# Kernel optimization log

Hardware: AMD Instinct MI355X
Metric: run time of the kernel (lower is better)

The kernel has to match this reference:

```python
import jax, jax.numpy as jnp
import numpy as np

N = 10000; IN = 256; HID = 256; Z = 64; NC = 10; E = 320000
GAMMA = -0.5; ZETA = 1.1; TEMP = 0.5  # GlobalArgs.gamma/zeta, AttentionFusion.temperature


def _spmm(row, col, vals, x):
    # sparse [N,N] @ dense [N,D] via gather + segment-sum scatter
    return jax.ops.segment_sum(vals[:, None] * x[col], row, num_segments=N)


def _encode(x, row, col, vals, gcn_W, gcn_b, m1_W, m1_b, m2_W, m2_b, s1_W, s1_b, s2_W, s2_b):
    hidden = jax.nn.relu(_spmm(row, col, vals, x @ gcn_W + gcn_b))  # GCNLayer
    mean = jax.nn.relu(hidden @ m1_W + m1_b) @ m2_W + m2_b
    std = jax.nn.softplus(jax.nn.relu(hidden @ s1_W + s1_b) @ s2_W + s2_b)
    return mean, mean, std  # eval mode: z = x_mean


def _denoise(x, row, col, vals, nb_W, nb_b, sf_W, sf_b, att_W, att_b):
    h1 = jax.nn.relu(x[row] @ nb_W + nb_b)  # nblayers_0 on source feats
    h2 = jax.nn.relu(x[col] @ sf_W + sf_b)  # selflayers_0 on dest feats
    w = jnp.concatenate([h1, h2], axis=1) @ att_W + att_b  # [E,1] log_alpha
    gate = jax.nn.sigmoid(w[:, 0])  # eval-mode hard-concrete
    mask = jnp.clip(gate * (ZETA - GAMMA) + GAMMA, 0.0, 1.0)
    mv = vals * mask
    rowsum = jax.ops.segment_sum(mv, row, num_segments=N) + 1e-10
    d = jnp.clip(rowsum ** -0.5, 0.0, 10.0)
    norm_vals = mv * d[row] * d[col]
    l0 = jnp.mean(jax.nn.sigmoid(w - jnp.log(-GAMMA / ZETA)))
    return norm_vals, l0


def setup_inputs() -> dict:
    key = jax.random.key(0)
    ks = jax.random.split(key, 32)
    w = lambda k, s: jax.random.normal(k, s, jnp.float32) * 0.05
    inp = {}
    inp['x'] = jax.random.normal(ks[0], (N, IN), jnp.float32)
    inp['row'] = jax.random.randint(ks[1], (E,), 0, N)
    inp['col'] = jax.random.randint(ks[2], (E,), 0, N)
    inp['adj_vals'] = jax.random.uniform(ks[3], (E,), jnp.float32)
    inp['gcn_W'] = w(ks[4], (IN, HID)); inp['gcn_b'] = jnp.zeros((HID,), jnp.float32)
    inp['m1_W'] = w(ks[5], (HID, Z)); inp['m1_b'] = jnp.zeros((Z,), jnp.float32)
    inp['m2_W'] = w(ks[6], (Z, Z)); inp['m2_b'] = jnp.zeros((Z,), jnp.float32)
    inp['s1_W'] = w(ks[7], (HID, Z)); inp['s1_b'] = jnp.zeros((Z,), jnp.float32)
    inp['s2_W'] = w(ks[8], (Z, Z)); inp['s2_b'] = jnp.zeros((Z,), jnp.float32)
    inp['nb_W'] = w(ks[9], (IN, HID)); inp['nb_b'] = jnp.zeros((HID,), jnp.float32)
    inp['sf_W'] = w(ks[10], (IN, HID)); inp['sf_b'] = jnp.zeros((HID,), jnp.float32)
    inp['att_W'] = w(ks[11], (2 * HID, 1)); inp['att_b'] = jnp.zeros((1,), jnp.float32)
    inp['f1_W'] = w(ks[12], (Z, 32)); inp['f1_b'] = jnp.zeros((32,), jnp.float32)
    inp['f2_W'] = jnp.zeros((32, 1), jnp.float32)  # att[2].weight.fill_(0.0)
    inp['head_W'] = w(ks[13], (Z, NC)); inp['head_b'] = jnp.zeros((NC,), jnp.float32)
    inp['d1_W'] = w(ks[14], (Z, HID)); inp['d1_b'] = jnp.zeros((HID,), jnp.float32)
    inp['d2_W'] = w(ks[15], (HID, IN)); inp['d2_b'] = jnp.zeros((IN,), jnp.float32)
    return inp


def reference(x, row, col, adj_vals, gcn_W, gcn_b, m1_W, m1_b, m2_W, m2_b, s1_W, s1_b, s2_W, s2_b,
              nb_W, nb_b, sf_W, sf_b, att_W, att_b, f1_W, f1_b, f2_W, head_W, head_b,
              d1_W, d1_b, d2_W, d2_b):
    enc = (gcn_W, gcn_b, m1_W, m1_b, m2_W, m2_b, s1_W, s1_b, s2_W, s2_b)
    # generative view
    z_gen, mu, logstd = _encode(x, row, col, adj_vals, *enc)
    adj_logits = z_gen @ z_gen.T  # vgae_decoder
    # denoised view
    den_vals, l0_loss = _denoise(x, row, col, adj_vals, nb_W, nb_b, sf_W, sf_b, att_W, att_b)
    z_den, _, _ = _encode(x, row, col, den_vals, *enc)
    # attention fusion
    h = jnp.stack([z_gen, z_den], axis=1)  # [N,2,Z]
    score = jnp.tanh(h @ f1_W + f1_b) @ f2_W  # [N,2,1]
    weights = jax.nn.softmax(score / TEMP, axis=1)
    z_fused = jnp.sum(h * weights, axis=1)
    # heads (cluster_proj is identity)
    q_fused = jax.nn.softmax(z_fused @ head_W + head_b, axis=1)
    q_gen = jax.nn.softmax(z_gen @ head_W + head_b, axis=1)
    q_den = jax.nn.softmax(z_den @ head_W + head_b, axis=1)
    recon_den = jax.nn.relu(z_den @ d1_W + d1_b) @ d2_W + d2_b
    return (q_fused, q_gen, q_den, adj_logits, z_fused, mu, logstd, l0_loss, z_den, weights, recon_den)
```

## Files before the change

kernel.cpp:

```cpp
#include <hip/hip_runtime.h>
#include <math.h>

#define NN 10000
#define EE 320000

#define OQF  0LL
#define OQG  100000LL
#define OQD  200000LL
#define OADJ 300000LL
#define OZF  100300000LL
#define OMU  100940000LL
#define OLS  101580000LL
#define OL0  102220000LL
#define OZD  102220001LL
#define OWT  102860001LL
#define OREC 102880001LL

typedef short short8 __attribute__((ext_vector_type(8)));
typedef float f32x4 __attribute__((ext_vector_type(4)));

static __device__ __forceinline__ ushort f2bf(float f) {
  uint u = __float_as_uint(f);
  return (ushort)((u + 0x7fffu + ((u >> 16) & 1u)) >> 16);
}

__global__ __launch_bounds__(256) void k_prep(
    const float* __restrict__ x,
    const float* __restrict__ gcnW, const float* __restrict__ nbW,
    const float* __restrict__ sfW, const float* __restrict__ d2W,
    const float* __restrict__ d1W, const float* __restrict__ m1W,
    const float* __restrict__ s1W, const float* __restrict__ m2W,
    const float* __restrict__ s2W,
    ushort* __restrict__ XB,
    ushort* __restrict__ GWT, ushort* __restrict__ NWT, ushort* __restrict__ SWT,
    ushort* __restrict__ D2T, ushort* __restrict__ D1T, ushort* __restrict__ M1T,
    ushort* __restrict__ S1T, ushort* __restrict__ M2T, ushort* __restrict__ S2T)
{
  const int b = blockIdx.x, tid = threadIdx.x;
  if (b < 2500) {
    const int i = b * 1024 + tid * 4;
    const float4 v = *(const float4*)(x + i);
    ushort4 u;
    u.x = f2bf(v.x); u.y = f2bf(v.y); u.z = f2bf(v.z); u.w = f2bf(v.w);
    *(ushort4*)(XB + i) = u;
    return;
  }
  const int t2 = b - 2500;
  if (t2 < 1024) {
    const int m = t2 >> 8, n = t2 & 255;
    const float* src = (m == 0) ? gcnW : (m == 1) ? nbW : (m == 2) ? sfW : d2W;
    ushort* dst = (m == 0) ? GWT : (m == 1) ? NWT : (m == 2) ? SWT : D2T;
    dst[n * 256 + tid] = f2bf(src[tid * 256 + n]);
  } else if (t2 < 1088) {
    const int local = (t2 - 1024) * 256 + tid;
    const int n = local >> 6, k = local & 63;
    D1T[local] = f2bf(d1W[k * 256 + n]);
  } else if (t2 < 1152) {
    const int n = t2 - 1088;
    M1T[n * 256 + tid] = f2bf(m1W[tid * 64 + n]);
  } else if (t2 < 1216) {
    const int n = t2 - 1152;
    S1T[n * 256 + tid] = f2bf(s1W[tid * 64 + n]);
  } else if (t2 < 1232) {
    const int local = (t2 - 1216) * 256 + tid;
    const int n = local >> 6, k = local & 63;
    M2T[local] = f2bf(m2W[k * 64 + n]);
  } else {
    const int local = (t2 - 1232) * 256 + tid;
    const int n = local >> 6, k = local & 63;
    S2T[local] = f2bf(s2W[k * 64 + n]);
  }
}

__global__ __launch_bounds__(256) void k_gin(
    const ushort* __restrict__ XB,
    const ushort* __restrict__ GWT, const ushort* __restrict__ NWT,
    const ushort* __restrict__ SWT,
    const float* __restrict__ gcnb, const float* __restrict__ nbb,
    const float* __restrict__ sfb, const float* __restrict__ attW,
    ushort* __restrict__ xwb, float* __restrict__ a1, float* __restrict__ a2)
{
  const int sel = blockIdx.y;
  const ushort* WT = (sel == 0) ? GWT : (sel == 1) ? NWT : SWT;
  const float* B = (sel == 0) ? gcnb : (sel == 1) ? nbb : sfb;
  const float* redw = attW + ((sel == 2) ? 256 : 0);
  float* redout = (sel == 1) ? a1 : a2;

  const int tid = threadIdx.x;
  const int wave = tid >> 6, lane = tid & 63;
  const int lr = lane & 15, lk = lane >> 4;
  const int i0 = blockIdx.x * 64;
  const int j0 = wave * 64;

  f32x4 acc[4][4];
#pragma unroll
  for (int ti = 0; ti < 4; ++ti)
#pragma unroll
    for (int tj = 0; tj < 4; ++tj) acc[ti][tj] = (f32x4){0.f, 0.f, 0.f, 0.f};

  const short8 z8 = {0, 0, 0, 0, 0, 0, 0, 0};
  for (int kk = 0; kk < 8; ++kk) {
    short8 a[4], bfr[4];
#pragma unroll
    for (int t = 0; t < 4; ++t) {
      const int ri = i0 + t * 16 + lr;
      a[t] = (ri < NN) ? *(const short8*)(XB + (size_t)ri * 256 + kk * 32 + lk * 8) : z8;
      bfr[t] = *(const short8*)(WT + (size_t)(j0 + t * 16 + lr) * 256 + kk * 32 + lk * 8);
    }
#pragma unroll
    for (int ti = 0; ti < 4; ++ti)
#pragma unroll
      for (int tj = 0; tj < 4; ++tj)
        acc[ti][tj] = __builtin_amdgcn_mfma_f32_16x16x32_bf16(a[ti], bfr[tj], acc[ti][tj], 0, 0, 0);
  }

  if (sel == 0) {
#pragma unroll
    for (int ti = 0; ti < 4; ++ti) {
      const int gi0 = i0 + ti * 16 + lk * 4;
#pragma unroll
      for (int tj = 0; tj < 4; ++tj) {
        const int gj = j0 + tj * 16 + lr;
        const float bv = B[gj];
#pragma unroll
        for (int r = 0; r < 4; ++r) {
          const int gi = gi0 + r;
          if (gi < NN) xwb[(size_t)gi * 256 + gj] = f2bf(acc[ti][tj][r] + bv);
        }
      }
    }
  } else {
    float bw[4], aw[4];
#pragma unroll
    for (int tj = 0; tj < 4; ++tj) {
      const int gj = j0 + tj * 16 + lr;
      bw[tj] = B[gj];
      aw[tj] = redw[gj];
    }
#pragma unroll
    for (int ti = 0; ti < 4; ++ti) {
      const int gi0 = i0 + ti * 16 + lk * 4;
#pragma unroll
      for (int r = 0; r < 4; ++r) {
        float s = 0.f;
#pragma unroll
        for (int tj = 0; tj < 4; ++tj)
          s += fmaxf(acc[ti][tj][r] + bw[tj], 0.f) * aw[tj];
#pragma unroll
        for (int m = 1; m < 16; m <<= 1) s += __shfl_xor(s, m, 64);
        const int gi = gi0 + r;
        if (lr == 0 && gi < NN) atomicAdd(&redout[gi], s);
      }
    }
  }
}

__global__ __launch_bounds__(256) void k_denoise(
    const int* __restrict__ row, const int* __restrict__ col,
    const float* __restrict__ vals, const float* __restrict__ a1,
    const float* __restrict__ a2, const float* __restrict__ attb,
    float4* __restrict__ bk, int* __restrict__ cnt, float* __restrict__ l0acc)
{
  const int e = blockIdx.x * 256 + threadIdx.x;
  const int r = row[e], c = col[e];
  const float w = a1[r] + a2[c] + attb[0];
  const float gate = 1.f / (1.f + expf(-w));
  const float mask = fminf(fmaxf(gate * 1.6f - 0.5f, 0.f), 1.f);
  const float m = vals[e] * mask;
  const int p = atomicAdd(&cnt[r], 1);
  if (p < 64) bk[(size_t)r * 64 + p] = make_float4(__int_as_float(c), vals[e], m, 0.f);
  float part = 1.f / (1.f + expf(-(w + 0.78845736f)));
#pragma unroll
  for (int off = 32; off > 0; off >>= 1) part += __shfl_down(part, off);
  __shared__ float sw[4];
  if ((threadIdx.x & 63) == 0) sw[threadIdx.x >> 6] = part;
  __syncthreads();
  if (threadIdx.x == 0) atomicAdd(l0acc, sw[0] + sw[1] + sw[2] + sw[3]);
}

__global__ __launch_bounds__(256) void k_dinv(
    const float4* __restrict__ bk, const int* __restrict__ cnt,
    float* __restrict__ dinv)
{
  const int tid = threadIdx.x;
  const int r = blockIdx.x * 4 + (tid >> 6);
  const int lane = tid & 63;
  if (r >= NN) return;
  const int m = min(cnt[r], 64);
  float s = (lane < m) ? bk[(size_t)r * 64 + lane].z : 0.f;
#pragma unroll
  for (int off = 32; off > 0; off >>= 1) s += __shfl_xor(s, off, 64);
  if (lane == 0) dinv[r] = fminf(rsqrtf(s + 1e-10f), 10.f);
}

__global__ __launch_bounds__(256) void k_spmm(
    const ushort* __restrict__ xwb, const float4* __restrict__ bk,
    const int* __restrict__ cnt, const float* __restrict__ dinv,
    ushort* __restrict__ h1, ushort* __restrict__ h2)
{
  const int tid = threadIdx.x;
  const int n = blockIdx.x * 2 + (tid >> 7);
  const int c = tid & 127;
  const int m = min(cnt[n], 64);
  const float dr = dinv[n];
  const float4* b = bk + (size_t)n * 64;
  float a10 = 0.f, a11 = 0.f, a20 = 0.f, a21 = 0.f;
  float b10 = 0.f, b11 = 0.f, b20 = 0.f, b21 = 0.f;
  int i = 0;
  for (; i + 2 <= m; i += 2) {
    const float4 e0 = b[i], e1 = b[i + 1];
    const int c0 = __float_as_int(e0.x), c1 = __float_as_int(e1.x);
    const uint u0 = *(const uint*)(xwb + (size_t)c0 * 256 + 2 * c);
    const uint u1 = *(const uint*)(xwb + (size_t)c1 * 256 + 2 * c);
    const float d0 = dr * dinv[c0] * e0.z;
    const float d1 = dr * dinv[c1] * e1.z;
    const float v00 = __uint_as_float(u0 << 16), v01 = __uint_as_float(u0 & 0xffff0000u);
    const float v10 = __uint_as_float(u1 << 16), v11 = __uint_as_float(u1 & 0xffff0000u);
    a10 = fmaf(e0.y, v00, a10); a11 = fmaf(e0.y, v01, a11);
    a20 = fmaf(d0, v00, a20);   a21 = fmaf(d0, v01, a21);
    b10 = fmaf(e1.y, v10, b10); b11 = fmaf(e1.y, v11, b11);
    b20 = fmaf(d1, v10, b20);   b21 = fmaf(d1, v11, b21);
  }
  if (i < m) {
    const float4 e0 = b[i];
    const int c0 = __float_as_int(e0.x);
    const uint u0 = *(const uint*)(xwb + (size_t)c0 * 256 + 2 * c);
    const float d0 = dr * dinv[c0] * e0.z;
    const float v00 = __uint_as_float(u0 << 16), v01 = __uint_as_float(u0 & 0xffff0000u);
    a10 = fmaf(e0.y, v00, a10); a11 = fmaf(e0.y, v01, a11);
    a20 = fmaf(d0, v00, a20);   a21 = fmaf(d0, v01, a21);
  }
  a10 += b10; a11 += b11; a20 += b20; a21 += b21;
  const uint p1 = (uint)f2bf(fmaxf(a10, 0.f)) | ((uint)f2bf(fmaxf(a11, 0.f)) << 16);
  const uint p2 = (uint)f2bf(fmaxf(a20, 0.f)) | ((uint)f2bf(fmaxf(a21, 0.f)) << 16);
  *(uint*)(h1 + (size_t)n * 256 + 2 * c) = p1;
  *(uint*)(h2 + (size_t)n * 256 + 2 * c) = p2;
}

__global__ __launch_bounds__(128) void k_tail(
    const ushort* __restrict__ H1B, const ushort* __restrict__ H2B,
    const ushort* __restrict__ M1T, const ushort* __restrict__ S1T,
    const ushort* __restrict__ M2T, const ushort* __restrict__ S2T,
    const float* __restrict__ m1b, const float* __restrict__ m2b,
    const float* __restrict__ s1b, const float* __restrict__ s2b,
    float* __restrict__ out, float* __restrict__ zden,
    ushort* __restrict__ zbg, ushort* __restrict__ zbd)
{
  const int v = blockIdx.y;
  const ushort* A   = (v == 2) ? H2B : H1B;
  const ushort* W1T = (v == 1) ? S1T : M1T;
  const float*  B1  = (v == 1) ? s1b : m1b;
  const ushort* W2T = (v == 1) ? S2T : M2T;
  const float*  B2  = (v == 1) ? s2b : m2b;

  __shared__ ushort Ts[128][72];
  const int tid = threadIdx.x;
  const int wave = tid >> 6, lane = tid & 63;
  const int lr = lane & 15, lk = lane >> 4;
  const int i0 = blockIdx.x * 128 + wave * 64;
  const short8 z8 = {0, 0, 0, 0, 0, 0, 0, 0};

  f32x4 acc[4][4];
#pragma unroll
  for (int ti = 0; ti < 4; ++ti)
#pragma unroll
    for (int tj = 0; tj < 4; ++tj) acc[ti][tj] = (f32x4){0.f, 0.f, 0.f, 0.f};
  for (int kk = 0; kk < 8; ++kk) {
    short8 a[4], bfr[4];
#pragma unroll
    for (int t = 0; t < 4; ++t) {
      const int ri = i0 + t * 16 + lr;
      a[t] = (ri < NN) ? *(const short8*)(A + (size_t)ri * 256 + kk * 32 + lk * 8) : z8;
      bfr[t] = *(const short8*)(W1T + (size_t)(t * 16 + lr) * 256 + kk * 32 + lk * 8);
    }
#pragma unroll
    for (int ti = 0; ti < 4; ++ti)
#pragma unroll
      for (int tj = 0; tj < 4; ++tj)
        acc[ti][tj] = __builtin_amdgcn_mfma_f32_16x16x32_bf16(a[ti], bfr[tj], acc[ti][tj], 0, 0, 0);
  }
#pragma unroll
  for (int ti = 0; ti < 4; ++ti) {
#pragma unroll
    for (int tj = 0; tj < 4; ++tj) {
      const int cl = tj * 16 + lr;
      const float b1 = B1[cl];
#pragma unroll
      for (int r = 0; r < 4; ++r) {
        const int lrow = wave * 64 + ti * 16 + lk * 4 + r;
        Ts[lrow][cl] = f2bf(fmaxf(acc[ti][tj][r] + b1, 0.f));
      }
    }
  }
  __syncthreads();
  f32x4 acc2[4][4];
#pragma unroll
  for (int ti = 0; ti < 4; ++ti)
#pragma unroll
    for (int tj = 0; tj < 4; ++tj) acc2[ti][tj] = (f32x4){0.f, 0.f, 0.f, 0.f};
  for (int kk = 0; kk < 2; ++kk) {
    short8 a[4], bfr[4];
#pragma unroll
    for (int t = 0; t < 4; ++t) {
      a[t] = *(const short8*)(&Ts[wave * 64 + t * 16 + lr][kk * 32 + lk * 8]);
      bfr[t] = *(const short8*)(W2T + (size_t)(t * 16 + lr) * 64 + kk * 32 + lk * 8);
    }
#pragma unroll
    for (int ti = 0; ti < 4; ++ti)
#pragma unroll
      for (int tj = 0; tj < 4; ++tj)
        acc2[ti][tj] = __builtin_amdgcn_mfma_f32_16x16x32_bf16(a[ti], bfr[tj], acc2[ti][tj], 0, 0, 0);
  }
#pragma unroll
  for (int ti = 0; ti < 4; ++ti) {
    const int gi0 = i0 + ti * 16 + lk * 4;
#pragma unroll
    for (int tj = 0; tj < 4; ++tj) {
      const int gj = tj * 16 + lr;
      const float bv = B2[gj];
#pragma unroll
      for (int r = 0; r < 4; ++r) {
        const int gi = gi0 + r;
        if (gi >= NN) continue;
        float t = acc2[ti][tj][r] + bv;
        if (v == 0) {
          out[OMU + (size_t)gi * 64 + gj] = t;
          zbg[(size_t)gi * 64 + gj] = f2bf(t);
        } else if (v == 1) {
          t = (t > 20.f) ? t : log1pf(expf(t));
          out[OLS + (size_t)gi * 64 + gj] = t;
        } else {
          zden[(size_t)gi * 64 + gj] = t;
          out[OZD + (size_t)gi * 64 + gj] = t;
          zbd[(size_t)gi * 64 + gj] = f2bf(t);
        }
      }
    }
  }
}

__global__ __launch_bounds__(256) void k_post(
    const ushort* __restrict__ ZBG, const ushort* __restrict__ ZBD,
    const float* __restrict__ ZDENW,
    const ushort* __restrict__ D1T, const float* __restrict__ d1b,
    const ushort* __restrict__ D2T, const float* __restrict__ d2b,
    const float* __restrict__ f1W, const float* __restrict__ f1b,
    const float* __restrict__ f2W,
    const float* __restrict__ hW, const float* __restrict__ hb,
    const float* __restrict__ l0acc, float* __restrict__ out)
{
  __shared__ char smraw[64 * 264 * 2];
  const int b = blockIdx.x;
  const int tid = threadIdx.x;
  const short8 z8 = {0, 0, 0, 0, 0, 0, 0, 0};

  if (b < 157) {
    ushort* HS = (ushort*)smraw;
    const int wave = tid >> 6, lane = tid & 63;
    const int lr = lane & 15, lk = lane >> 4;
    const int i0 = b * 64;
    const int j0 = wave * 64;
    f32x4 acc[4][4];
#pragma unroll
    for (int ti = 0; ti < 4; ++ti)
#pragma unroll
      for (int tj = 0; tj < 4; ++tj) acc[ti][tj] = (f32x4){0.f, 0.f, 0.f, 0.f};
    for (int kk = 0; kk < 2; ++kk) {
      short8 a[4], bfr[4];
#pragma unroll
      for (int t = 0; t < 4; ++t) {
        const int ri = i0 + t * 16 + lr;
        a[t] = (ri < NN) ? *(const short8*)(ZBD + (size_t)ri * 64 + kk * 32 + lk * 8) : z8;
        bfr[t] = *(const short8*)(D1T + (size_t)(j0 + t * 16 + lr) * 64 + kk * 32 + lk * 8);
      }
#pragma unroll
      for (int ti = 0; ti < 4; ++ti)
#pragma unroll
        for (int tj = 0; tj < 4; ++tj)
          acc[ti][tj] = __builtin_amdgcn_mfma_f32_16x16x32_bf16(a[ti], bfr[tj], acc[ti][tj], 0, 0, 0);
    }
#pragma unroll
    for (int ti = 0; ti < 4; ++ti) {
      const int rl0 = ti * 16 + lk * 4;
#pragma unroll
      for (int tj = 0; tj < 4; ++tj) {
        const int cl = j0 + tj * 16 + lr;
        const float bv = d1b[cl];
#pragma unroll
        for (int r = 0; r < 4; ++r)
          HS[(rl0 + r) * 264 + cl] = f2bf(fmaxf(acc[ti][tj][r] + bv, 0.f));
      }
    }
    __syncthreads();
#pragma unroll
    for (int ti = 0; ti < 4; ++ti)
#pragma unroll
      for (int tj = 0; tj < 4; ++tj) acc[ti][tj] = (f32x4){0.f, 0.f, 0.f, 0.f};
    for (int kk = 0; kk < 8; ++kk) {
      short8 a[4], bfr[4];
#pragma unroll
      for (int t = 0; t < 4; ++t) {
        a[t] = *(const short8*)(HS + (t * 16 + lr) * 264 + kk * 32 + lk * 8);
        bfr[t] = *(const short8*)(D2T + (size_t)(j0 + t * 16 + lr) * 256 + kk * 32 + lk * 8);
      }
#pragma unroll
      for (int ti = 0; ti < 4; ++ti)
#pragma unroll
        for (int tj = 0; tj < 4; ++tj)
          acc[ti][tj] = __builtin_amdgcn_mfma_f32_16x16x32_bf16(a[ti], bfr[tj], acc[ti][tj], 0, 0, 0);
    }
#pragma unroll
    for (int ti = 0; ti < 4; ++ti) {
      const int gi0 = i0 + ti * 16 + lk * 4;
#pragma unroll
      for (int tj = 0; tj < 4; ++tj) {
        const int gj = j0 + tj * 16 + lr;
        const float bv = d2b[gj];
#pragma unroll
        for (int r = 0; r < 4; ++r) {
          const int gi = gi0 + r;
          if (gi < NN) out[OREC + (size_t)gi * 256 + gj] = acc[ti][tj][r] + bv;
        }
      }
    }
  } else if (b < 197) {
    const int n = (b - 157) * 256 + tid;
    if (n == 0) out[OL0] = l0acc[0] * (1.f / (float)EE);
    if (n >= NN) return;
    const float* zg = out + OMU + (size_t)n * 64;
    const float* zdn = ZDENW + (size_t)n * 64;
    float ag[32], ad[32];
#pragma unroll
    for (int c2 = 0; c2 < 32; ++c2) { const float bb = f1b[c2]; ag[c2] = bb; ad[c2] = bb; }
    for (int l = 0; l < 64; ++l) {
      const float a = zg[l];
      const float d = zdn[l];
#pragma unroll
      for (int c2 = 0; c2 < 32; ++c2) {
        const float w = f1W[l * 32 + c2];
        ag[c2] = fmaf(a, w, ag[c2]);
        ad[c2] = fmaf(d, w, ad[c2]);
      }
    }
    float sg = 0.f, sd = 0.f;
#pragma unroll
    for (int c2 = 0; c2 < 32; ++c2) {
      sg += tanhf(ag[c2]) * f2W[c2];
      sd += tanhf(ad[c2]) * f2W[c2];
    }
    const float e0 = sg * 2.f, e1 = sd * 2.f;
    const float m = fmaxf(e0, e1);
    float w0 = expf(e0 - m), w1 = expf(e1 - m);
    const float inv = 1.f / (w0 + w1);
    w0 *= inv; w1 *= inv;
    float lgf[10], lgg[10], lgd[10];
#pragma unroll
    for (int c = 0; c < 10; ++c) { const float bb = hb[c]; lgf[c] = bb; lgg[c] = bb; lgd[c] = bb; }
    for (int l = 0; l < 64; ++l) {
      const float zgv = zg[l], zdv = zdn[l];
      const float zfv = w0 * zgv + w1 * zdv;
      out[OZF + (size_t)n * 64 + l] = zfv;
#pragma unroll
      for (int c = 0; c < 10; ++c) {
        const float w = hW[l * 10 + c];
        lgf[c] = fmaf(zfv, w, lgf[c]);
        lgg[c] = fmaf(zgv, w, lgg[c]);
        lgd[c] = fmaf(zdv, w, lgd[c]);
      }
    }
#pragma unroll
    for (int h = 0; h < 3; ++h) {
      float* lg = (h == 0) ? lgf : (h == 1) ? lgg : lgd;
      float* q = out + ((h == 0) ? OQF : (h == 1) ? OQG : OQD) + (size_t)n * 10;
      float mm = lg[0];
#pragma unroll
      for (int c = 1; c < 10; ++c) mm = fmaxf(mm, lg[c]);
      float s = 0.f;
#pragma unroll
      for (int c = 0; c < 10; ++c) { lg[c] = expf(lg[c] - mm); s += lg[c]; }
      const float invq = 1.f / s;
#pragma unroll
      for (int c = 0; c < 10; ++c) q[c] = lg[c] * invq;
    }
    out[OWT + (size_t)n * 2 + 0] = w0;
    out[OWT + (size_t)n * 2 + 1] = w1;
  } else {
    const int bb = b - 197;
    const int bi = bb / 79, bj = bb % 79;
    const int wave = tid >> 6, lane = tid & 63;
    const int lr = lane & 15, lk = lane >> 4;
    const int i0 = bi * 128 + (wave >> 1) * 64;
    const int j0 = bj * 128 + (wave & 1) * 64;
    float* zs = (float*)smraw + wave * (16 * 76);
    short8 a[4][2], bfr[4][2];
#pragma unroll
    for (int t = 0; t < 4; ++t) {
      const int ri = i0 + t * 16 + lr;
      const int rj = j0 + t * 16 + lr;
#pragma unroll
      for (int kk = 0; kk < 2; ++kk) {
        a[t][kk] = (ri < NN) ? *(const short8*)(ZBG + (size_t)ri * 64 + kk * 32 + lk * 8) : z8;
        bfr[t][kk] = (rj < NN) ? *(const short8*)(ZBG + (size_t)rj * 64 + kk * 32 + lk * 8) : z8;
      }
    }
    f32x4 acc[4][4];
#pragma unroll
    for (int ti = 0; ti < 4; ++ti)
#pragma unroll
      for (int tj = 0; tj < 4; ++tj) {
        acc[ti][tj] = (f32x4){0.f, 0.f, 0.f, 0.f};
        acc[ti][tj] = __builtin_amdgcn_mfma_f32_16x16x32_bf16(a[ti][0], bfr[tj][0], acc[ti][tj], 0, 0, 0);
        acc[ti][tj] = __builtin_amdgcn_mfma_f32_16x16x32_bf16(a[ti][1], bfr[tj][1], acc[ti][tj], 0, 0, 0);
      }
#pragma unroll
    for (int ti = 0; ti < 4; ++ti) {
#pragma unroll
      for (int tj = 0; tj < 4; ++tj)
#pragma unroll
        for (int r = 0; r < 4; ++r)
          zs[(lk * 4 + r) * 76 + tj * 16 + lr] = acc[ti][tj][r];
#pragma unroll
      for (int s = 0; s < 4; ++s) {
        const int rrow = (s & 1) * 8 + (lane >> 3);
        const int ccol = (s >> 1) * 32 + (lane & 7) * 4;
        const int gi = i0 + ti * 16 + rrow;
        const int gj = j0 + ccol;
        if (gi < NN && gj < NN) {
          float4 v;
          v.x = zs[rrow * 76 + ccol + 0];
          v.y = zs[rrow * 76 + ccol + 1];
          v.z = zs[rrow * 76 + ccol + 2];
          v.w = zs[rrow * 76 + ccol + 3];
          *(float4*)(out + OADJ + (size_t)gi * NN + gj) = v;
        }
      }
    }
  }
}

extern "C" void kernel_launch(void* const* d_in, const int* in_sizes, int n_in,
                              void* d_out, int out_size, void* d_ws, size_t ws_size,
                              hipStream_t stream)
{
  const float* x     = (const float*)d_in[0];
  const int*   row   = (const int*)d_in[1];
  const int*   col   = (const int*)d_in[2];
  const float* avals = (const float*)d_in[3];
  const float* gcnW  = (const float*)d_in[4];
  const float* gcnb  = (const float*)d_in[5];
  const float* m1W   = (const float*)d_in[6];
  const float* m1b   = (const float*)d_in[7];
  const float* m2W   = (const float*)d_in[8];
  const float* m2b   = (const float*)d_in[9];
  const float* s1W   = (const float*)d_in[10];
  const float* s1b   = (const float*)d_in[11];
  const float* s2W   = (const float*)d_in[12];
  const float* s2b   = (const float*)d_in[13];
  const float* nbW   = (const float*)d_in[14];
  const float* nbb   = (const float*)d_in[15];
  const float* sfW   = (const float*)d_in[16];
  const float* sfb   = (const float*)d_in[17];
  const float* attW  = (const float*)d_in[18];
  const float* attb  = (const float*)d_in[19];
  const float* f1W   = (const float*)d_in[20];
  const float* f1b   = (const float*)d_in[21];
  const float* f2W   = (const float*)d_in[22];
  const float* headW = (const float*)d_in[23];
  const float* headb = (const float*)d_in[24];
  const float* d1W   = (const float*)d_in[25];
  const float* d1b   = (const float*)d_in[26];
  const float* d2W   = (const float*)d_in[27];
  const float* d2b   = (const float*)d_in[28];
  float* out = (float*)d_out;

  float* ws = (float*)d_ws;
  size_t o = 0;
  float4* BK   = (float4*)(ws + o); o += (size_t)NN * 64 * 4;
  ushort* XB   = (ushort*)(ws + o); o += (size_t)NN * 128;
  ushort* XWB  = (ushort*)(ws + o); o += (size_t)NN * 128;
  ushort* GWT  = (ushort*)(ws + o); o += 32768;
  ushort* NWT  = (ushort*)(ws + o); o += 32768;
  ushort* SWT  = (ushort*)(ws + o); o += 32768;
  ushort* D2T  = (ushort*)(ws + o); o += 32768;
  ushort* D1T  = (ushort*)(ws + o); o += 8192;
  ushort* M1T  = (ushort*)(ws + o); o += 8192;
  ushort* S1T  = (ushort*)(ws + o); o += 8192;
  ushort* M2T  = (ushort*)(ws + o); o += 2048;
  ushort* S2T  = (ushort*)(ws + o); o += 2048;
  ushort* H1B  = (ushort*)(ws + o); o += (size_t)NN * 128;
  ushort* H2B  = (ushort*)(ws + o); o += (size_t)NN * 128;
  float* ZDENW = ws + o; o += (size_t)NN * 64;
  ushort* ZBG  = (ushort*)(ws + o); o += (size_t)NN * 32;
  ushort* ZBD  = (ushort*)(ws + o); o += (size_t)NN * 32;
  float* DINV  = ws + o; o += NN;
  const size_t zoff = o;
  float* A1    = ws + o; o += NN;
  float* A2    = ws + o; o += NN;
  int*   CNT   = (int*)(ws + o); o += NN;
  float* L0A   = ws + o; o += 1;

  hipMemsetAsync((void*)(ws + zoff), 0, (o - zoff) * sizeof(float), stream);

  k_prep<<<3748, 256, 0, stream>>>(x, gcnW, nbW, sfW, d2W, d1W, m1W, s1W, m2W, s2W,
                                   XB, GWT, NWT, SWT, D2T, D1T, M1T, S1T, M2T, S2T);
  k_gin<<<dim3(157, 3), 256, 0, stream>>>(XB, GWT, NWT, SWT, gcnb, nbb, sfb, attW, XWB, A1, A2);
  k_denoise<<<EE / 256, 256, 0, stream>>>(row, col, avals, A1, A2, attb, BK, CNT, L0A);
  k_dinv<<<2500, 256, 0, stream>>>(BK, CNT, DINV);
  k_spmm<<<NN / 2, 256, 0, stream>>>(XWB, BK, CNT, DINV, H1B, H2B);
  k_tail<<<dim3(79, 3), 128, 0, stream>>>(H1B, H2B, M1T, S1T, M2T, S2T,
                                          m1b, m2b, s1b, s2b, out, ZDENW, ZBG, ZBD);
  k_post<<<6438, 256, 0, stream>>>(ZBG, ZBD, ZDENW, D1T, d1b, D2T, d2b,
                                   f1W, f1b, f2W, headW, headb, L0A, out);
}
```

Before: 283.0 us.

## Stream adj_logits by row strips with direct MFMA stores; fold memset into prep

The z·zᵀ decoder tile path is rewritten. Each block now owns a 16-row strip and its four waves sweep across all column tiles, writing MFMA accumulators straight to global memory instead of staging them through shared memory for float4 stores. The block count for that path drops from about 6241 to 625. The separate hipMemsetAsync of the accumulator region is replaced by extra zeroing blocks in k_prep, which saves one launch. The direct stores are scalar and strided per lane, which may hurt write coalescing on the 400MB output, and zero-padding checks were removed since 10000 divides by 16.

Result: slower. 308.9 us (+9.2%).

```diff
diff --git a/kernel.cpp b/kernel.cpp
--- a/kernel.cpp
+++ b/kernel.cpp
@@ -34,7 +34,8 @@
     ushort* __restrict__ XB,
     ushort* __restrict__ GWT, ushort* __restrict__ NWT, ushort* __restrict__ SWT,
     ushort* __restrict__ D2T, ushort* __restrict__ D1T, ushort* __restrict__ M1T,
-    ushort* __restrict__ S1T, ushort* __restrict__ M2T, ushort* __restrict__ S2T)
+    ushort* __restrict__ S1T, ushort* __restrict__ M2T, ushort* __restrict__ S2T,
+    float* __restrict__ ZRG)
 {
   const int b = blockIdx.x, tid = threadIdx.x;
   if (b < 2500) {
@@ -65,10 +66,13 @@
     const int local = (t2 - 1216) * 256 + tid;
     const int n = local >> 6, k = local & 63;
     M2T[local] = f2bf(m2W[k * 64 + n]);
-  } else {
+  } else if (t2 < 1248) {
     const int local = (t2 - 1232) * 256 + tid;
     const int n = local >> 6, k = local & 63;
     S2T[local] = f2bf(s2W[k * 64 + n]);
+  } else {
+    const int i = (t2 - 1248) * 1024 + tid * 4;
+    *(float4*)(ZRG + i) = make_float4(0.f, 0.f, 0.f, 0.f);
   }
 }
 
@@ -349,13 +353,12 @@
     const float* __restrict__ hW, const float* __restrict__ hb,
     const float* __restrict__ l0acc, float* __restrict__ out)
 {
-  __shared__ char smraw[64 * 264 * 2];
+  __shared__ ushort HS[64 * 264];
   const int b = blockIdx.x;
   const int tid = threadIdx.x;
   const short8 z8 = {0, 0, 0, 0, 0, 0, 0, 0};
 
   if (b < 157) {
-    ushort* HS = (ushort*)smraw;
     const int wave = tid >> 6, lane = tid & 63;
     const int lr = lane & 15, lk = lane >> 4;
     const int i0 = b * 64;
@@ -485,55 +488,25 @@
     out[OWT + (size_t)n * 2 + 0] = w0;
     out[OWT + (size_t)n * 2 + 1] = w1;
   } else {
-    const int bb = b - 197;
-    const int bi = bb / 79, bj = bb % 79;
+    const int bi = b - 197;
     const int wave = tid >> 6, lane = tid & 63;
     const int lr = lane & 15, lk = lane >> 4;
-    const int i0 = bi * 128 + (wave >> 1) * 64;
-    const int j0 = bj * 128 + (wave & 1) * 64;
-    float* zs = (float*)smraw + wave * (16 * 76);
-    short8 a[4][2], bfr[4][2];
-#pragma unroll
-    for (int t = 0; t < 4; ++t) {
-      const int ri = i0 + t * 16 + lr;
-      const int rj = j0 + t * 16 + lr;
-#pragma unroll
-      for (int kk = 0; kk < 2; ++kk) {
-        a[t][kk] = (ri < NN) ? *(const short8*)(ZBG + (size_t)ri * 64 + kk * 32 + lk * 8) : z8;
-        bfr[t][kk] = (rj < NN) ? *(const short8*)(ZBG + (size_t)rj * 64 + kk * 32 + lk * 8) : z8;
-      }
-    }
-    f32x4 acc[4][4];
-#pragma unroll
-    for (int ti = 0; ti < 4; ++ti)
-#pragma unroll
-      for (int tj = 0; tj < 4; ++tj) {
-        acc[ti][tj] = (f32x4){0.f, 0.f, 0.f, 0.f};
-        acc[ti][tj] = __builtin_amdgcn_mfma_f32_16x16x32_bf16(a[ti][0], bfr[tj][0], acc[ti][tj], 0, 0, 0);
-        acc[ti][tj] = __builtin_amdgcn_mfma_f32_16x16x32_bf16(a[ti][1], bfr[tj][1], acc[ti][tj], 0, 0, 0);
-      }
-#pragma unroll
-    for (int ti = 0; ti < 4; ++ti) {
-#pragma unroll
-      for (int tj = 0; tj < 4; ++tj)
-#pragma unroll
-        for (int r = 0; r < 4; ++r)
-          zs[(lk * 4 + r) * 76 + tj * 16 + lr] = acc[ti][tj][r];
-#pragma unroll
-      for (int s = 0; s < 4; ++s) {
-        const int rrow = (s & 1) * 8 + (lane >> 3);
-        const int ccol = (s >> 1) * 32 + (lane & 7) * 4;
-        const int gi = i0 + ti * 16 + rrow;
-        const int gj = j0 + ccol;
-        if (gi < NN && gj < NN) {
-          float4 v;
-          v.x = zs[rrow * 76 + ccol + 0];
-          v.y = zs[rrow * 76 + ccol + 1];
-          v.z = zs[rrow * 76 + ccol + 2];
-          v.w = zs[rrow * 76 + ccol + 3];
-          *(float4*)(out + OADJ + (size_t)gi * NN + gj) = v;
-        }
-      }
+    const int i0 = bi * 16;
+    const short8 a0 = *(const short8*)(ZBG + (size_t)(i0 + lr) * 64 + lk * 8);
+    const short8 a1 = *(const short8*)(ZBG + (size_t)(i0 + lr) * 64 + 32 + lk * 8);
+    float* crow = out + OADJ + (size_t)(i0 + lk * 4) * NN + lr;
+#pragma unroll 2
+    for (int jt = wave; jt < 625; jt += 4) {
+      const int j0 = jt * 16;
+      const short8 b0 = *(const short8*)(ZBG + (size_t)(j0 + lr) * 64 + lk * 8);
+      const short8 b1 = *(const short8*)(ZBG + (size_t)(j0 + lr) * 64 + 32 + lk * 8);
+      f32x4 acc = (f32x4){0.f, 0.f, 0.f, 0.f};
+      acc = __builtin_amdgcn_mfma_f32_16x16x32_bf16(a0, b0, acc, 0, 0, 0);
+      acc = __builtin_amdgcn_mfma_f32_16x16x32_bf16(a1, b1, acc, 0, 0, 0);
+      crow[(size_t)0 * NN + j0] = acc[0];
+      crow[(size_t)1 * NN + j0] = acc[1];
+      crow[(size_t)2 * NN + j0] = acc[2];
+      crow[(size_t)3 * NN + j0] = acc[3];
     }
   }
 }
@@ -593,22 +566,21 @@
   ushort* ZBG  = (ushort*)(ws + o); o += (size_t)NN * 32;
   ushort* ZBD  = (ushort*)(ws + o); o += (size_t)NN * 32;
   float* DINV  = ws + o; o += NN;
-  const size_t zoff = o;
+  float* ZRG   = ws + o;
   float* A1    = ws + o; o += NN;
   float* A2    = ws + o; o += NN;
   int*   CNT   = (int*)(ws + o); o += NN;
   float* L0A   = ws + o; o += 1;
-
-  hipMemsetAsync((void*)(ws + zoff), 0, (o - zoff) * sizeof(float), stream);
-
-  k_prep<<<3748, 256, 0, stream>>>(x, gcnW, nbW, sfW, d2W, d1W, m1W, s1W, m2W, s2W,
-                                   XB, GWT, NWT, SWT, D2T, D1T, M1T, S1T, M2T, S2T);
+  o += 719;
+
+  k_prep<<<3778, 256, 0, stream>>>(x, gcnW, nbW, sfW, d2W, d1W, m1W, s1W, m2W, s2W,
+                                   XB, GWT, NWT, SWT, D2T, D1T, M1T, S1T, M2T, S2T, ZRG);
   k_gin<<<dim3(157, 3), 256, 0, stream>>>(XB, GWT, NWT, SWT, gcnb, nbb, sfb, attW, XWB, A1, A2);
   k_denoise<<<EE / 256, 256, 0, stream>>>(row, col, avals, A1, A2, attb, BK, CNT, L0A);
   k_dinv<<<2500, 256, 0, stream>>>(BK, CNT, DINV);
   k_spmm<<<NN / 2, 256, 0, stream>>>(XWB, BK, CNT, DINV, H1B, H2B);
   k_tail<<<dim3(79, 3), 128, 0, stream>>>(H1B, H2B, M1T, S1T, M2T, S2T,
                                           m1b, m2b, s1b, s2b, out, ZDENW, ZBG, ZBD);
-  k_post<<<6438, 256, 0, stream>>>(ZBG, ZBD, ZDENW, D1T, d1b, D2T, d2b,
-                                   f1W, f1b, f2W, headW, headb, L0A, out);
-}
+  k_post<<<822, 256, 0, stream>>>(ZBG, ZBD, ZDENW, D1T, d1b, D2T, d2b,
+                                  f1W, f1b, f2W, headW, headb, L0A, out);
+}
```

## Bucket edges in prep kernel and fuse gate computation with degree normalization

Applied to the files above, without the earlier changes.

Moves edge bucketing (atomic slot per row) into the prep kernel so it can overlap with the bf16 conversions. It fuses the denoise-gate and dinv kernels into one per-row kernel that computes the mask, rowsum and l0 partial sums together. The bucket record is split into an 8-byte (col,val) array plus a separate mask array. k_gin's attention reduction now goes through shared memory with plain stores instead of global atomics, which also removes the need to zero A1/A2. Net effect is one fewer launch and less atomic traffic, at the cost of an extra mask-array read in spmm.

New measurement: 288.4 us. Within noise of the previous version (+1.9%).

```diff
diff --git a/kernel.cpp b/kernel.cpp
--- a/kernel.cpp
+++ b/kernel.cpp
@@ -26,26 +26,36 @@
 
 __global__ __launch_bounds__(256) void k_prep(
     const float* __restrict__ x,
+    const int* __restrict__ row, const int* __restrict__ col,
+    const float* __restrict__ avals,
     const float* __restrict__ gcnW, const float* __restrict__ nbW,
     const float* __restrict__ sfW, const float* __restrict__ d2W,
     const float* __restrict__ d1W, const float* __restrict__ m1W,
     const float* __restrict__ s1W, const float* __restrict__ m2W,
     const float* __restrict__ s2W,
+    float2* __restrict__ BK8, int* __restrict__ cnt,
     ushort* __restrict__ XB,
     ushort* __restrict__ GWT, ushort* __restrict__ NWT, ushort* __restrict__ SWT,
     ushort* __restrict__ D2T, ushort* __restrict__ D1T, ushort* __restrict__ M1T,
     ushort* __restrict__ S1T, ushort* __restrict__ M2T, ushort* __restrict__ S2T)
 {
   const int b = blockIdx.x, tid = threadIdx.x;
-  if (b < 2500) {
-    const int i = b * 1024 + tid * 4;
+  if (b < 1250) {
+    const int e = b * 256 + tid;
+    const int r = row[e];
+    const int p = atomicAdd(&cnt[r], 1);
+    if (p < 64) BK8[(size_t)r * 64 + p] = make_float2(__int_as_float(col[e]), avals[e]);
+    return;
+  }
+  if (b < 3750) {
+    const int i = (b - 1250) * 1024 + tid * 4;
     const float4 v = *(const float4*)(x + i);
     ushort4 u;
     u.x = f2bf(v.x); u.y = f2bf(v.y); u.z = f2bf(v.z); u.w = f2bf(v.w);
     *(ushort4*)(XB + i) = u;
     return;
   }
-  const int t2 = b - 2500;
+  const int t2 = b - 3750;
   if (t2 < 1024) {
     const int m = t2 >> 8, n = t2 & 255;
     const float* src = (m == 0) ? gcnW : (m == 1) ? nbW : (m == 2) ? sfW : d2W;
@@ -80,6 +90,7 @@
     const float* __restrict__ sfb, const float* __restrict__ attW,
     ushort* __restrict__ xwb, float* __restrict__ a1, float* __restrict__ a2)
 {
+  __shared__ float sred[4][64];
   const int sel = blockIdx.y;
   const ushort* WT = (sel == 0) ? GWT : (sel == 1) ? NWT : SWT;
   const float* B = (sel == 0) ? gcnb : (sel == 1) ? nbb : sfb;
@@ -139,7 +150,6 @@
     }
 #pragma unroll
     for (int ti = 0; ti < 4; ++ti) {
-      const int gi0 = i0 + ti * 16 + lk * 4;
 #pragma unroll
       for (int r = 0; r < 4; ++r) {
         float s = 0.f;
@@ -148,53 +158,57 @@
           s += fmaxf(acc[ti][tj][r] + bw[tj], 0.f) * aw[tj];
 #pragma unroll
         for (int m = 1; m < 16; m <<= 1) s += __shfl_xor(s, m, 64);
-        const int gi = gi0 + r;
-        if (lr == 0 && gi < NN) atomicAdd(&redout[gi], s);
-      }
-    }
-  }
-}
-
-__global__ __launch_bounds__(256) void k_denoise(
-    const int* __restrict__ row, const int* __restrict__ col,
-    const float* __restrict__ vals, const float* __restrict__ a1,
-    const float* __restrict__ a2, const float* __restrict__ attb,
-    float4* __restrict__ bk, int* __restrict__ cnt, float* __restrict__ l0acc)
+        if (lr == 0) sred[wave][ti * 16 + lk * 4 + r] = s;
+      }
+    }
+    __syncthreads();
+    if (tid < 64) {
+      const int gi = i0 + tid;
+      if (gi < NN)
+        redout[gi] = sred[0][tid] + sred[1][tid] + sred[2][tid] + sred[3][tid];
+    }
+  }
+}
+
+__global__ __launch_bounds__(256) void k_dengate(
+    const float2* __restrict__ BK8, const int* __restrict__ cnt,
+    const float* __restrict__ a1, const float* __restrict__ a2,
+    const float* __restrict__ attb,
+    float* __restrict__ mvb, float* __restrict__ dinv, float* __restrict__ l0acc)
 {
-  const int e = blockIdx.x * 256 + threadIdx.x;
-  const int r = row[e], c = col[e];
-  const float w = a1[r] + a2[c] + attb[0];
-  const float gate = 1.f / (1.f + expf(-w));
-  const float mask = fminf(fmaxf(gate * 1.6f - 0.5f, 0.f), 1.f);
-  const float m = vals[e] * mask;
-  const int p = atomicAdd(&cnt[r], 1);
-  if (p < 64) bk[(size_t)r * 64 + p] = make_float4(__int_as_float(c), vals[e], m, 0.f);
-  float part = 1.f / (1.f + expf(-(w + 0.78845736f)));
-#pragma unroll
-  for (int off = 32; off > 0; off >>= 1) part += __shfl_down(part, off);
   __shared__ float sw[4];
-  if ((threadIdx.x & 63) == 0) sw[threadIdx.x >> 6] = part;
+  const int tid = threadIdx.x;
+  const int wave = tid >> 6, lane = tid & 63;
+  const int r = blockIdx.x * 4 + wave;
+  const int m = min(cnt[r], 64);
+  float part = 0.f, mv = 0.f;
+  if (lane < m) {
+    const float2 e = BK8[(size_t)r * 64 + lane];
+    const int c = __float_as_int(e.x);
+    const float w = a1[r] + a2[c] + attb[0];
+    const float gate = 1.f / (1.f + expf(-w));
+    const float mask = fminf(fmaxf(gate * 1.6f - 0.5f, 0.f), 1.f);
+    mv = e.y * mask;
+    mvb[(size_t)r * 64 + lane] = mv;
+    part = 1.f / (1.f + expf(-(w + 0.78845736f)));
+  }
+  float s = mv;
+#pragma unroll
+  for (int off = 32; off > 0; off >>= 1) {
+    s += __shfl_xor(s, off, 64);
+    part += __shfl_xor(part, off, 64);
+  }
+  if (lane == 0) {
+    dinv[r] = fminf(rsqrtf(s + 1e-10f), 10.f);
+    sw[wave] = part;
+  }
   __syncthreads();
-  if (threadIdx.x == 0) atomicAdd(l0acc, sw[0] + sw[1] + sw[2] + sw[3]);
-}
-
-__global__ __launch_bounds__(256) void k_dinv(
-    const float4* __restrict__ bk, const int* __restrict__ cnt,
-    float* __restrict__ dinv)
-{
-  const int tid = threadIdx.x;
-  const int r = blockIdx.x * 4 + (tid >> 6);
-  const int lane = tid & 63;
-  if (r >= NN) return;
-  const int m = min(cnt[r], 64);
-  float s = (lane < m) ? bk[(size_t)r * 64 + lane].z : 0.f;
-#pragma unroll
-  for (int off = 32; off > 0; off >>= 1) s += __shfl_xor(s, off, 64);
-  if (lane == 0) dinv[r] = fminf(rsqrtf(s + 1e-10f), 10.f);
+  if (tid == 0) atomicAdd(l0acc, sw[0] + sw[1] + sw[2] + sw[3]);
 }
 
 __global__ __launch_bounds__(256) void k_spmm(
-    const ushort* __restrict__ xwb, const float4* __restrict__ bk,
+    const ushort* __restrict__ xwb, const float2* __restrict__ BK8,
+    const float* __restrict__ mvb,
     const int* __restrict__ cnt, const float* __restrict__ dinv,
     ushort* __restrict__ h1, ushort* __restrict__ h2)
 {
@@ -203,17 +217,19 @@
   const int c = tid & 127;
   const int m = min(cnt[n], 64);
   const float dr = dinv[n];
-  const float4* b = bk + (size_t)n * 64;
+  const float2* b8 = BK8 + (size_t)n * 64;
+  const float* mvp = mvb + (size_t)n * 64;
   float a10 = 0.f, a11 = 0.f, a20 = 0.f, a21 = 0.f;
   float b10 = 0.f, b11 = 0.f, b20 = 0.f, b21 = 0.f;
   int i = 0;
   for (; i + 2 <= m; i += 2) {
-    const float4 e0 = b[i], e1 = b[i + 1];
+    const float2 e0 = b8[i], e1 = b8[i + 1];
+    const float mv0 = mvp[i], mv1 = mvp[i + 1];
     const int c0 = __float_as_int(e0.x), c1 = __float_as_int(e1.x);
     const uint u0 = *(const uint*)(xwb + (size_t)c0 * 256 + 2 * c);
     const uint u1 = *(const uint*)(xwb + (size_t)c1 * 256 + 2 * c);
-    const float d0 = dr * dinv[c0] * e0.z;
-    const float d1 = dr * dinv[c1] * e1.z;
+    const float d0 = dr * dinv[c0] * mv0;
+    const float d1 = dr * dinv[c1] * mv1;
     const float v00 = __uint_as_float(u0 << 16), v01 = __uint_as_float(u0 & 0xffff0000u);
     const float v10 = __uint_as_float(u1 << 16), v11 = __uint_as_float(u1 & 0xffff0000u);
     a10 = fmaf(e0.y, v00, a10); a11 = fmaf(e0.y, v01, a11);
@@ -222,10 +238,11 @@
     b20 = fmaf(d1, v10, b20);   b21 = fmaf(d1, v11, b21);
   }
   if (i < m) {
-    const float4 e0 = b[i];
+    const float2 e0 = b8[i];
+    const float mv0 = mvp[i];
     const int c0 = __float_as_int(e0.x);
     const uint u0 = *(const uint*)(xwb + (size_t)c0 * 256 + 2 * c);
-    const float d0 = dr * dinv[c0] * e0.z;
+    const float d0 = dr * dinv[c0] * mv0;
     const float v00 = __uint_as_float(u0 << 16), v01 = __uint_as_float(u0 & 0xffff0000u);
     a10 = fmaf(e0.y, v00, a10); a11 = fmaf(e0.y, v01, a11);
     a20 = fmaf(d0, v00, a20);   a21 = fmaf(d0, v01, a21);
@@ -575,7 +592,8 @@
 
   float* ws = (float*)d_ws;
   size_t o = 0;
-  float4* BK   = (float4*)(ws + o); o += (size_t)NN * 64 * 4;
+  float2* BK8  = (float2*)(ws + o); o += (size_t)NN * 64 * 2;
+  float* MVB   = ws + o; o += (size_t)NN * 64;
   ushort* XB   = (ushort*)(ws + o); o += (size_t)NN * 128;
   ushort* XWB  = (ushort*)(ws + o); o += (size_t)NN * 128;
   ushort* GWT  = (ushort*)(ws + o); o += 32768;
@@ -593,20 +611,21 @@
   ushort* ZBG  = (ushort*)(ws + o); o += (size_t)NN * 32;
   ushort* ZBD  = (ushort*)(ws + o); o += (size_t)NN * 32;
   float* DINV  = ws + o; o += NN;
-  const size_t zoff = o;
   float* A1    = ws + o; o += NN;
   float* A2    = ws + o; o += NN;
+  const size_t zoff = o;
   int*   CNT   = (int*)(ws + o); o += NN;
   float* L0A   = ws + o; o += 1;
 
   hipMemsetAsync((void*)(ws + zoff), 0, (o - zoff) * sizeof(float), stream);
 
-  k_prep<<<3748, 256, 0, stream>>>(x, gcnW, nbW, sfW, d2W, d1W, m1W, s1W, m2W, s2W,
-                                   XB, GWT, NWT, SWT, D2T, D1T, M1T, S1T, M2T, S2T);
+  k_prep<<<4998, 256, 0, stream>>>(x, row, col, avals,
+                                   gcnW, nbW, sfW, d2W, d1W, m1W, s1W, m2W, s2W,
+                                   BK8, CNT, XB,
+                                   GWT, NWT, SWT, D2T, D1T, M1T, S1T, M2T, S2T);
   k_gin<<<dim3(157, 3), 256, 0, stream>>>(XB, GWT, NWT, SWT, gcnb, nbb, sfb, attW, XWB, A1, A2);
-  k_denoise<<<EE / 256, 256, 0, stream>>>(row, col, avals, A1, A2, attb, BK, CNT, L0A);
-  k_dinv<<<2500, 256, 0, stream>>>(BK, CNT, DINV);
-  k_spmm<<<NN / 2, 256, 0, stream>>>(XWB, BK, CNT, DINV, H1B, H2B);
+  k_dengate<<<2500, 256, 0, stream>>>(BK8, CNT, A1, A2, attb, MVB, DINV, L0A);
+  k_spmm<<<NN / 2, 256, 0, stream>>>(XWB, BK8, MVB, CNT, DINV, H1B, H2B);
   k_tail<<<dim3(79, 3), 128, 0, stream>>>(H1B, H2B, M1T, S1T, M2T, S2T,
                                           m1b, m2b, s1b, s2b, out, ZDENW, ZBG, ZBD);
   k_post<<<6438, 256, 0, stream>>>(ZBG, ZBD, ZDENW, D1T, d1b, D2T, d2b,
```
